# Optimization experiments

Measured on AMD Instinct MI355X. Metric: run time of the kernel, lower is better.

The kernel has to match this reference:

```python
import jax, jax.numpy as jnp
import numpy as np

KERNEL_MUL = 2.0
KERNEL_NUM = 5
EPS = 1e-5


def _gaussian_kernel(a, b):
    # a: [n, d], b: [m, d]. Squared L2 distances via dot-product trick
    # (same math as the tiled (n,m,d) subtraction in the original, without
    # materializing the rank-3 intermediate).
    sq_a = jnp.sum(a * a, axis=1)  # [n]
    sq_b = jnp.sum(b * b, axis=1)  # [m]
    d2 = sq_a[:, None] + sq_b[None, :] - 2.0 * (a @ b.T)  # [n, m]
    d2 = jnp.maximum(d2, 0.0)
    n_samples = a.shape[0] + b.shape[0]
    # bandwidth from detached distances (L2_distance.data in torch)
    bw = jax.lax.stop_gradient(jnp.sum(d2)) / (n_samples ** 2 - n_samples)
    bw = bw / (KERNEL_MUL ** (KERNEL_NUM // 2))
    bws = bw * (KERNEL_MUL ** jnp.arange(KERNEL_NUM, dtype=d2.dtype)) + EPS  # [K]
    # sum of K Gaussian kernels, fused over the bandwidth axis
    k = jnp.sum(jnp.exp(-d2[None, :, :] / bws[:, None, None]), axis=0)  # [n, m]
    return k


def setup_inputs() -> dict:
    key = jax.random.key(0)
    kx, ky = jax.random.split(key)
    x = jax.random.normal(kx, (4096, 256), dtype=jnp.float32)
    y = jax.random.normal(ky, (4096, 256), dtype=jnp.float32)
    return {"x": x, "y": y}


def reference(x, y):
    xx = _gaussian_kernel(x, x).mean()
    yy = _gaussian_kernel(y, y).mean()
    xy = _gaussian_kernel(x, y).mean()
    mmd = xx + yy - 2.0 * xy
    return mmd
```

## Files before the change

kernel.cpp:

```cpp
#include <hip/hip_runtime.h>

#define N 4096
#define D 256
#define BT 128
#define NB2 32
#define TRI 528
#define TOTAL 2080
#define BK 32
#define KT (D / BK)

typedef __attribute__((ext_vector_type(8))) _Float16 f16x8;
typedef __attribute__((ext_vector_type(4))) _Float16 f16x4;
typedef __attribute__((ext_vector_type(4))) float f32x4;

__device__ __forceinline__ void gld_lds16(const void* g, void* l) {
    __builtin_amdgcn_global_load_lds(
        (const __attribute__((address_space(1))) unsigned int*)g,
        (__attribute__((address_space(3))) unsigned int*)l, 16, 0, 0);
}

__global__ void k_cvt(const float* __restrict__ x, const float* __restrict__ y,
                      _Float16* __restrict__ xc, _Float16* __restrict__ yc,
                      float* __restrict__ sq, double* __restrict__ cs) {
    const int mat = blockIdx.y;
    const float* src = mat ? y : x;
    _Float16* dst = mat ? yc : xc;
    const int w = threadIdx.x >> 6, lane = threadIdx.x & 63;
    const int r0 = blockIdx.x * 32 + w * 8;
    __shared__ float lds[4][256];
    float4 colacc = {0.f, 0.f, 0.f, 0.f};
    #pragma unroll
    for (int r = 0; r < 8; ++r) {
        const int row = r0 + r;
        const float4 v = *(const float4*)(src + (size_t)row * D + lane * 4);
        f16x4 h;
        h.x = (_Float16)v.x; h.y = (_Float16)v.y;
        h.z = (_Float16)v.z; h.w = (_Float16)v.w;
        *(f16x4*)(dst + (size_t)row * D + lane * 4) = h;
        float s = v.x * v.x + v.y * v.y + v.z * v.z + v.w * v.w;
        #pragma unroll
        for (int off = 32; off; off >>= 1) s += __shfl_down(s, off);
        if (lane == 0) sq[mat * N + row] = s;
        colacc.x += v.x; colacc.y += v.y; colacc.z += v.z; colacc.w += v.w;
    }
    *(float4*)&lds[w][lane * 4] = colacc;
    __syncthreads();
    const int t = threadIdx.x;
    const float part = lds[0][t] + lds[1][t] + lds[2][t] + lds[3][t];
    atomicAdd(&cs[mat * D + t], (double)part);
}

__global__ void k_prep(const float* __restrict__ sq, const double* __restrict__ cs,
                       float* __restrict__ coef, double* __restrict__ acc) {
    const int t = threadIdx.x;
    double sx = 0, sy = 0;
    for (int i = t; i < N; i += 256) { sx += (double)sq[i]; sy += (double)sq[N + i]; }
    const double cx = cs[t], cy = cs[D + t];
    double v[5] = {sx, sy, cx * cx, cy * cy, cx * cy};
    #pragma unroll
    for (int k = 0; k < 5; ++k)
        for (int off = 32; off; off >>= 1) v[k] += __shfl_down(v[k], off);
    __shared__ double red[4][5];
    const int w = t >> 6, lane = t & 63;
    if (lane == 0) for (int k = 0; k < 5; ++k) red[w][k] = v[k];
    __syncthreads();
    if (t == 0) {
        double Sx = 0, Sy = 0, Cxx = 0, Cyy = 0, Cxy = 0;
        for (int q = 0; q < 4; ++q) {
            Sx += red[q][0]; Sy += red[q][1];
            Cxx += red[q][2]; Cyy += red[q][3]; Cxy += red[q][4];
        }
        const double ns = 2.0 * N;
        const double denom = ns * ns - ns;
        const double sd[3] = {
            2.0 * N * Sx - 2.0 * Cxx,
            2.0 * N * Sy - 2.0 * Cyy,
            (double)N * Sx + (double)N * Sy - 2.0 * Cxy };
        const double L2E = 1.4426950408889634;
        for (int q = 0; q < 3; ++q) {
            const double bw = sd[q] / denom / 4.0;
            coef[q] = (float)(L2E / (16.0 * bw + 1e-5));
        }
        acc[0] = 0.0; acc[1] = 0.0; acc[2] = 0.0;
    }
}

__global__ __launch_bounds__(256) void k_mmd(
    const _Float16* __restrict__ xc, const _Float16* __restrict__ yc,
    const float* __restrict__ sq, const float* __restrict__ coefs,
    double* __restrict__ acc) {
    __shared__ __align__(16) _Float16 As[2 * BT * BK];
    __shared__ __align__(16) _Float16 Bs[2 * BT * BK];
    __shared__ double red[4];

    const int bid = (blockIdx.x & 7) * (TOTAL / 8) + (blockIdx.x >> 3);

    int p, b;
    if (bid < TRI)          { p = 0; b = bid; }
    else if (bid < 2 * TRI) { p = 1; b = bid - TRI; }
    else                    { p = 2; b = bid - 2 * TRI; }
    const _Float16* A = (p == 1) ? yc : xc;
    const _Float16* B = (p == 0) ? xc : yc;
    const float* sqA = (p == 1) ? sq + N : sq;
    const float* sqB = (p == 0) ? sq : sq + N;
    const float c4 = coefs[p];

    int bi, bj;
    if (p < 2) {
        int rem = b, r = 0;
        while (rem >= NB2 - r) { rem -= NB2 - r; ++r; }
        bi = r; bj = r + rem;
    } else { bi = b >> 5; bj = b & 31; }

    const int tid = threadIdx.x;
    const int srow = tid >> 2;
    const int sc = (tid & 3) ^ (srow & 3) ^ ((srow >> 2) & 3);
    const char* gA = (const char*)A + (size_t)(bi * BT + srow) * (D * 2) + sc * 16;
    const char* gB = (const char*)B + (size_t)(bj * BT + srow) * (D * 2) + sc * 16;
    char* lA = (char*)As + tid * 16;
    char* lB = (char*)Bs + tid * 16;

    const int lane = tid & 63, w = tid >> 6;
    const int wr = (w >> 1) * 64, wc = (w & 1) * 64;
    const int fr = lane & 15;
    const int lg = lane >> 4;
    const int ch = (lg ^ (fr & 3) ^ (fr >> 2)) * 16;
    const char* rA = (const char*)As + (wr + fr) * 64 + ch;
    const char* rB = (const char*)Bs + (wc + fr) * 64 + ch;

    f32x4 accv[4][4];
    #pragma unroll
    for (int m = 0; m < 4; ++m)
        #pragma unroll
        for (int n = 0; n < 4; ++n) accv[m][n] = {0.f, 0.f, 0.f, 0.f};

    gld_lds16(gA, lA);
    gld_lds16(gA + 64 * (D * 2), lA + 4096);
    gld_lds16(gB, lB);
    gld_lds16(gB + 64 * (D * 2), lB + 4096);
    __syncthreads();

    #pragma unroll
    for (int kt = 0; kt < KT; ++kt) {
        const int c = kt & 1;
        if (kt + 1 < KT) {
            const int kb = (kt + 1) * (BK * 2);
            const int co = (c ^ 1) * 8192;
            gld_lds16(gA + kb, lA + co);
            gld_lds16(gA + kb + 64 * (D * 2), lA + co + 4096);
            gld_lds16(gB + kb, lB + co);
            gld_lds16(gB + kb + 64 * (D * 2), lB + co + 4096);
        }
        const int co = c * 8192;
        f16x8 af[4], bf[4];
        #pragma unroll
        for (int m = 0; m < 4; ++m)
            af[m] = *(const f16x8*)(rA + co + m * 1024);
        #pragma unroll
        for (int n = 0; n < 4; ++n)
            bf[n] = *(const f16x8*)(rB + co + n * 1024);
        #pragma unroll
        for (int m = 0; m < 4; ++m)
            #pragma unroll
            for (int n = 0; n < 4; ++n)
                accv[m][n] = __builtin_amdgcn_mfma_f32_16x16x32_f16(
                    af[m], bf[n], accv[m][n], 0, 0, 0);
        if (kt + 1 < KT) __syncthreads();
    }

    const float c2x = 2.f * c4;
    const int row0 = bi * BT + wr + lg * 4;
    const int col0 = bj * BT + wc + fr;
    float asa[4][4], bsb[4];
    #pragma unroll
    for (int m = 0; m < 4; ++m) {
        const f32x4 sa = *(const f32x4*)(sqA + row0 + m * 16);
        #pragma unroll
        for (int i = 0; i < 4; ++i) asa[m][i] = sa[i] * c4;
    }
    #pragma unroll
    for (int n = 0; n < 4; ++n) bsb[n] = sqB[col0 + n * 16] * c4;
    float s = 0.f;
    #pragma unroll
    for (int m = 0; m < 4; ++m)
        #pragma unroll
        for (int n = 0; n < 4; ++n)
            #pragma unroll
            for (int i = 0; i < 4; ++i) {
                float arg = fmaf(accv[m][n][i], c2x, -(asa[m][i] + bsb[n]));
                arg = fminf(arg, 0.f);
                const float u = __builtin_amdgcn_exp2f(arg);
                const float u2 = u * u, u4 = u2 * u2;
                const float u8 = u4 * u4, u16 = u8 * u8;
                s += (u + u2) + (u4 + u8) + u16;
            }
    if (p < 2 && bi != bj) s *= 2.f;

    double sd = (double)s;
    #pragma unroll
    for (int off = 32; off; off >>= 1) sd += __shfl_down(sd, off);
    if (lane == 0) red[w] = sd;
    __syncthreads();
    if (tid == 0) atomicAdd(&acc[p], red[0] + red[1] + red[2] + red[3]);
}

__global__ void k_final(const double* __restrict__ acc, float* __restrict__ out) {
    const double inv = 1.0 / ((double)N * (double)N);
    out[0] = (float)((acc[0] + acc[1] - 2.0 * acc[2]) * inv);
}

extern "C" void kernel_launch(void* const* d_in, const int* in_sizes, int n_in,
                              void* d_out, int out_size, void* d_ws, size_t ws_size,
                              hipStream_t stream) {
    const float* x = (const float*)d_in[0];
    const float* y = (const float*)d_in[1];
    float* out = (float*)d_out;

    double* wsd = (double*)d_ws;
    double* acc = wsd;
    double* cs  = wsd + 8;
    float*  sq  = (float*)(wsd + 520);
    float*  coef = sq + 2 * N;
    char* base = (char*)d_ws;
    _Float16* xc = (_Float16*)(base + 40960);
    _Float16* yc = (_Float16*)(base + 40960 + (size_t)N * D * 2);

    hipMemsetAsync(cs, 0, 512 * sizeof(double), stream);
    k_cvt<<<dim3(N / 32, 2), 256, 0, stream>>>(x, y, xc, yc, sq, cs);
    k_prep<<<1, 256, 0, stream>>>(sq, cs, coef, acc);
    k_mmd<<<TOTAL, 256, 0, stream>>>(xc, yc, sq, coef, acc);
    k_final<<<1, 1, 0, stream>>>(acc, out);
}
```

Measured before the change: 116.2 us.

## Fuse bandwidth prep into MMD kernel and deepen LDS prefetch pipeline

```diff
diff --git a/kernel.cpp b/kernel.cpp
--- a/kernel.cpp
+++ b/kernel.cpp
@@ -50,50 +50,15 @@
     atomicAdd(&cs[mat * D + t], (double)part);
 }
 
-__global__ void k_prep(const float* __restrict__ sq, const double* __restrict__ cs,
-                       float* __restrict__ coef, double* __restrict__ acc) {
-    const int t = threadIdx.x;
-    double sx = 0, sy = 0;
-    for (int i = t; i < N; i += 256) { sx += (double)sq[i]; sy += (double)sq[N + i]; }
-    const double cx = cs[t], cy = cs[D + t];
-    double v[5] = {sx, sy, cx * cx, cy * cy, cx * cy};
-    #pragma unroll
-    for (int k = 0; k < 5; ++k)
-        for (int off = 32; off; off >>= 1) v[k] += __shfl_down(v[k], off);
-    __shared__ double red[4][5];
-    const int w = t >> 6, lane = t & 63;
-    if (lane == 0) for (int k = 0; k < 5; ++k) red[w][k] = v[k];
-    __syncthreads();
-    if (t == 0) {
-        double Sx = 0, Sy = 0, Cxx = 0, Cyy = 0, Cxy = 0;
-        for (int q = 0; q < 4; ++q) {
-            Sx += red[q][0]; Sy += red[q][1];
-            Cxx += red[q][2]; Cyy += red[q][3]; Cxy += red[q][4];
-        }
-        const double ns = 2.0 * N;
-        const double denom = ns * ns - ns;
-        const double sd[3] = {
-            2.0 * N * Sx - 2.0 * Cxx,
-            2.0 * N * Sy - 2.0 * Cyy,
-            (double)N * Sx + (double)N * Sy - 2.0 * Cxy };
-        const double L2E = 1.4426950408889634;
-        for (int q = 0; q < 3; ++q) {
-            const double bw = sd[q] / denom / 4.0;
-            coef[q] = (float)(L2E / (16.0 * bw + 1e-5));
-        }
-        acc[0] = 0.0; acc[1] = 0.0; acc[2] = 0.0;
-    }
-}
-
 __global__ __launch_bounds__(256) void k_mmd(
     const _Float16* __restrict__ xc, const _Float16* __restrict__ yc,
-    const float* __restrict__ sq, const float* __restrict__ coefs,
+    const float* __restrict__ sq, const double* __restrict__ cs,
     double* __restrict__ acc) {
     __shared__ __align__(16) _Float16 As[2 * BT * BK];
     __shared__ __align__(16) _Float16 Bs[2 * BT * BK];
     __shared__ double red[4];
 
-    const int bid = (blockIdx.x & 7) * (TOTAL / 8) + (blockIdx.x >> 3);
+    const int bid = blockIdx.x;
 
     int p, b;
     if (bid < TRI)          { p = 0; b = bid; }
@@ -103,7 +68,6 @@
     const _Float16* B = (p == 0) ? xc : yc;
     const float* sqA = (p == 1) ? sq + N : sq;
     const float* sqB = (p == 0) ? sq : sq + N;
-    const float c4 = coefs[p];
 
     int bi, bj;
     if (p < 2) {
@@ -113,6 +77,8 @@
     } else { bi = b >> 5; bj = b & 31; }
 
     const int tid = threadIdx.x;
+    const int lane = tid & 63, w = tid >> 6;
+
     const int srow = tid >> 2;
     const int sc = (tid & 3) ^ (srow & 3) ^ ((srow >> 2) & 3);
     const char* gA = (const char*)A + (size_t)(bi * BT + srow) * (D * 2) + sc * 16;
@@ -120,7 +86,49 @@
     char* lA = (char*)As + tid * 16;
     char* lB = (char*)Bs + tid * 16;
 
-    const int lane = tid & 63, w = tid >> 6;
+#define STAGE(kt, buf) do { \
+        const int kb_ = (kt) * (BK * 2); const int co_ = (buf) * 8192; \
+        gld_lds16(gA + kb_, lA + co_); \
+        gld_lds16(gA + kb_ + 64 * (D * 2), lA + co_ + 4096); \
+        gld_lds16(gB + kb_, lB + co_); \
+        gld_lds16(gB + kb_ + 64 * (D * 2), lB + co_ + 4096); \
+    } while (0)
+
+    STAGE(0, 0);
+    STAGE(1, 1);
+
+    float c4;
+    {
+        double sx = 0, sy = 0;
+        for (int i = lane * 4; i < N; i += 256) {
+            const float4 a = *(const float4*)(sq + i);
+            const float4 c = *(const float4*)(sq + N + i);
+            sx += (double)a.x + (double)a.y + (double)a.z + (double)a.w;
+            sy += (double)c.x + (double)c.y + (double)c.z + (double)c.w;
+        }
+        double cxx = 0, cyy = 0, cxy = 0;
+        for (int j = lane; j < D; j += 64) {
+            const double cx = cs[j], cy = cs[D + j];
+            cxx += cx * cx; cyy += cy * cy; cxy += cx * cy;
+        }
+        #pragma unroll
+        for (int off = 32; off; off >>= 1) {
+            sx += __shfl_xor(sx, off);  sy += __shfl_xor(sy, off);
+            cxx += __shfl_xor(cxx, off); cyy += __shfl_xor(cyy, off);
+            cxy += __shfl_xor(cxy, off);
+        }
+        const double ns = 2.0 * N;
+        const double denom = ns * ns - ns;
+        double sd;
+        if (p == 0)      sd = 2.0 * N * sx - 2.0 * cxx;
+        else if (p == 1) sd = 2.0 * N * sy - 2.0 * cyy;
+        else             sd = (double)N * sx + (double)N * sy - 2.0 * cxy;
+        const double bw = sd / denom / 4.0;
+        c4 = (float)(1.4426950408889634 / (16.0 * bw + 1e-5));
+    }
+    asm volatile("" : "+v"(c4));
+    __builtin_amdgcn_sched_barrier(0);
+
     const int wr = (w >> 1) * 64, wc = (w & 1) * 64;
     const int fr = lane & 15;
     const int lg = lane >> 4;
@@ -134,24 +142,13 @@
         #pragma unroll
         for (int n = 0; n < 4; ++n) accv[m][n] = {0.f, 0.f, 0.f, 0.f};
 
-    gld_lds16(gA, lA);
-    gld_lds16(gA + 64 * (D * 2), lA + 4096);
-    gld_lds16(gB, lB);
-    gld_lds16(gB + 64 * (D * 2), lB + 4096);
-    __syncthreads();
-
     #pragma unroll
     for (int kt = 0; kt < KT; ++kt) {
-        const int c = kt & 1;
-        if (kt + 1 < KT) {
-            const int kb = (kt + 1) * (BK * 2);
-            const int co = (c ^ 1) * 8192;
-            gld_lds16(gA + kb, lA + co);
-            gld_lds16(gA + kb + 64 * (D * 2), lA + co + 4096);
-            gld_lds16(gB + kb, lB + co);
-            gld_lds16(gB + kb + 64 * (D * 2), lB + co + 4096);
-        }
-        const int co = c * 8192;
+        if (kt < KT - 1) asm volatile("s_waitcnt vmcnt(4)" ::: "memory");
+        else             asm volatile("s_waitcnt vmcnt(0)" ::: "memory");
+        __builtin_amdgcn_s_barrier();
+        __builtin_amdgcn_sched_barrier(0);
+        const int co = (kt & 1) * 8192;
         f16x8 af[4], bf[4];
         #pragma unroll
         for (int m = 0; m < 4; ++m)
@@ -165,7 +162,10 @@
             for (int n = 0; n < 4; ++n)
                 accv[m][n] = __builtin_amdgcn_mfma_f32_16x16x32_f16(
                     af[m], bf[n], accv[m][n], 0, 0, 0);
-        if (kt + 1 < KT) __syncthreads();
+        asm volatile("s_waitcnt lgkmcnt(0)" ::: "memory");
+        __builtin_amdgcn_s_barrier();
+        __builtin_amdgcn_sched_barrier(0);
+        if (kt + 2 < KT) STAGE(kt + 2, kt & 1);
     }
 
     const float c2x = 2.f * c4;
@@ -202,6 +202,7 @@
     if (lane == 0) red[w] = sd;
     __syncthreads();
     if (tid == 0) atomicAdd(&acc[p], red[0] + red[1] + red[2] + red[3]);
+#undef STAGE
 }
 
 __global__ void k_final(const double* __restrict__ acc, float* __restrict__ out) {
@@ -220,14 +221,12 @@
     double* acc = wsd;
     double* cs  = wsd + 8;
     float*  sq  = (float*)(wsd + 520);
-    float*  coef = sq + 2 * N;
     char* base = (char*)d_ws;
     _Float16* xc = (_Float16*)(base + 40960);
     _Float16* yc = (_Float16*)(base + 40960 + (size_t)N * D * 2);
 
-    hipMemsetAsync(cs, 0, 512 * sizeof(double), stream);
+    hipMemsetAsync(wsd, 0, 520 * sizeof(double), stream);
     k_cvt<<<dim3(N / 32, 2), 256, 0, stream>>>(x, y, xc, yc, sq, cs);
-    k_prep<<<1, 256, 0, stream>>>(sq, cs, coef, acc);
-    k_mmd<<<TOTAL, 256, 0, stream>>>(xc, yc, sq, coef, acc);
+    k_mmd<<<TOTAL, 256, 0, stream>>>(xc, yc, sq, cs, acc);
     k_final<<<1, 1, 0, stream>>>(acc, out);
 }
```

Result: slower. 126.7 us (+9.1%).

## Drop column-sum atomics and memset; hand-place waitcnt/barriers in GEMM loop

Applied to the files above, without the earlier changes.

```diff
diff --git a/kernel.cpp b/kernel.cpp
--- a/kernel.cpp
+++ b/kernel.cpp
@@ -21,7 +21,7 @@
 
 __global__ void k_cvt(const float* __restrict__ x, const float* __restrict__ y,
                       _Float16* __restrict__ xc, _Float16* __restrict__ yc,
-                      float* __restrict__ sq, double* __restrict__ cs) {
+                      float* __restrict__ sq, float* __restrict__ pb) {
     const int mat = blockIdx.y;
     const float* src = mat ? y : x;
     _Float16* dst = mat ? yc : xc;
@@ -46,16 +46,20 @@
     *(float4*)&lds[w][lane * 4] = colacc;
     __syncthreads();
     const int t = threadIdx.x;
-    const float part = lds[0][t] + lds[1][t] + lds[2][t] + lds[3][t];
-    atomicAdd(&cs[mat * D + t], (double)part);
-}
-
-__global__ void k_prep(const float* __restrict__ sq, const double* __restrict__ cs,
+    pb[(mat * (N / 32) + blockIdx.x) * 256 + t] =
+        lds[0][t] + lds[1][t] + lds[2][t] + lds[3][t];
+}
+
+__global__ void k_prep(const float* __restrict__ sq, const float* __restrict__ pb,
                        float* __restrict__ coef, double* __restrict__ acc) {
     const int t = threadIdx.x;
     double sx = 0, sy = 0;
     for (int i = t; i < N; i += 256) { sx += (double)sq[i]; sy += (double)sq[N + i]; }
-    const double cx = cs[t], cy = cs[D + t];
+    double cx = 0, cy = 0;
+    for (int b = 0; b < N / 32; ++b) {
+        cx += (double)pb[b * 256 + t];
+        cy += (double)pb[(N / 32 + b) * 256 + t];
+    }
     double v[5] = {sx, sy, cx * cx, cy * cy, cx * cy};
     #pragma unroll
     for (int k = 0; k < 5; ++k)
@@ -113,6 +117,8 @@
     } else { bi = b >> 5; bj = b & 31; }
 
     const int tid = threadIdx.x;
+    const int lane = tid & 63, w = tid >> 6;
+
     const int srow = tid >> 2;
     const int sc = (tid & 3) ^ (srow & 3) ^ ((srow >> 2) & 3);
     const char* gA = (const char*)A + (size_t)(bi * BT + srow) * (D * 2) + sc * 16;
@@ -120,7 +126,14 @@
     char* lA = (char*)As + tid * 16;
     char* lB = (char*)Bs + tid * 16;
 
-    const int lane = tid & 63, w = tid >> 6;
+#define STAGE(kt, buf) do { \
+        const int kb_ = (kt) * (BK * 2); const int co_ = (buf) * 8192; \
+        gld_lds16(gA + kb_, lA + co_); \
+        gld_lds16(gA + kb_ + 64 * (D * 2), lA + co_ + 4096); \
+        gld_lds16(gB + kb_, lB + co_); \
+        gld_lds16(gB + kb_ + 64 * (D * 2), lB + co_ + 4096); \
+    } while (0)
+
     const int wr = (w >> 1) * 64, wc = (w & 1) * 64;
     const int fr = lane & 15;
     const int lg = lane >> 4;
@@ -134,24 +147,15 @@
         #pragma unroll
         for (int n = 0; n < 4; ++n) accv[m][n] = {0.f, 0.f, 0.f, 0.f};
 
-    gld_lds16(gA, lA);
-    gld_lds16(gA + 64 * (D * 2), lA + 4096);
-    gld_lds16(gB, lB);
-    gld_lds16(gB + 64 * (D * 2), lB + 4096);
-    __syncthreads();
+    STAGE(0, 0);
+    asm volatile("s_waitcnt vmcnt(0)" ::: "memory");
+    __builtin_amdgcn_s_barrier();
+    __builtin_amdgcn_sched_barrier(0);
 
     #pragma unroll
     for (int kt = 0; kt < KT; ++kt) {
-        const int c = kt & 1;
-        if (kt + 1 < KT) {
-            const int kb = (kt + 1) * (BK * 2);
-            const int co = (c ^ 1) * 8192;
-            gld_lds16(gA + kb, lA + co);
-            gld_lds16(gA + kb + 64 * (D * 2), lA + co + 4096);
-            gld_lds16(gB + kb, lB + co);
-            gld_lds16(gB + kb + 64 * (D * 2), lB + co + 4096);
-        }
-        const int co = c * 8192;
+        if (kt + 1 < KT) STAGE(kt + 1, (kt + 1) & 1);
+        const int co = (kt & 1) * 8192;
         f16x8 af[4], bf[4];
         #pragma unroll
         for (int m = 0; m < 4; ++m)
@@ -159,13 +163,19 @@
         #pragma unroll
         for (int n = 0; n < 4; ++n)
             bf[n] = *(const f16x8*)(rB + co + n * 1024);
+        asm volatile("s_waitcnt lgkmcnt(0)" ::: "memory");
+        __builtin_amdgcn_sched_barrier(0);
         #pragma unroll
         for (int m = 0; m < 4; ++m)
             #pragma unroll
             for (int n = 0; n < 4; ++n)
                 accv[m][n] = __builtin_amdgcn_mfma_f32_16x16x32_f16(
                     af[m], bf[n], accv[m][n], 0, 0, 0);
-        if (kt + 1 < KT) __syncthreads();
+        if (kt + 1 < KT) {
+            asm volatile("s_waitcnt vmcnt(0)" ::: "memory");
+            __builtin_amdgcn_s_barrier();
+            __builtin_amdgcn_sched_barrier(0);
+        }
     }
 
     const float c2x = 2.f * c4;
@@ -202,6 +212,7 @@
     if (lane == 0) red[w] = sd;
     __syncthreads();
     if (tid == 0) atomicAdd(&acc[p], red[0] + red[1] + red[2] + red[3]);
+#undef STAGE
 }
 
 __global__ void k_final(const double* __restrict__ acc, float* __restrict__ out) {
@@ -216,18 +227,16 @@
     const float* y = (const float*)d_in[1];
     float* out = (float*)d_out;
 
-    double* wsd = (double*)d_ws;
-    double* acc = wsd;
-    double* cs  = wsd + 8;
-    float*  sq  = (float*)(wsd + 520);
-    float*  coef = sq + 2 * N;
     char* base = (char*)d_ws;
-    _Float16* xc = (_Float16*)(base + 40960);
-    _Float16* yc = (_Float16*)(base + 40960 + (size_t)N * D * 2);
-
-    hipMemsetAsync(cs, 0, 512 * sizeof(double), stream);
-    k_cvt<<<dim3(N / 32, 2), 256, 0, stream>>>(x, y, xc, yc, sq, cs);
-    k_prep<<<1, 256, 0, stream>>>(sq, cs, coef, acc);
+    double* acc = (double*)base;
+    float*  sq  = (float*)(base + 64);
+    float*  coef = (float*)(base + 64 + 32768);
+    float*  pb  = (float*)(base + 65536);
+    _Float16* xc = (_Float16*)(base + 65536 + 262144);
+    _Float16* yc = (_Float16*)(base + 65536 + 262144 + N * D * 2);
+
+    k_cvt<<<dim3(N / 32, 2), 256, 0, stream>>>(x, y, xc, yc, sq, pb);
+    k_prep<<<1, 256, 0, stream>>>(sq, pb, coef, acc);
     k_mmd<<<TOTAL, 256, 0, stream>>>(xc, yc, sq, coef, acc);
     k_final<<<1, 1, 0, stream>>>(acc, out);
 }
```

Result: slower. 119.7 us (+3.0%).
